# Performance work log

Hardware: AMD Instinct MI355X
Metric: run time of the kernel (lower is better)

Reference implementation:

```python
import jax, jax.numpy as jnp
import numpy as np

ALPHA = 0.9        # synaptic decay (hidden layers; layer 0 uses 0*syn + h)
BETA = 0.85        # membrane leak
THRESHOLD = 1.0
SIM_TIME = 50
SCALE = 100.0      # SurrGradSpike.scale


@jax.custom_vjp
def spike_fn(x):
    # Heaviside step: 1.0 where x > 0 (strict, matching torch `input > 0`)
    return (x > 0).astype(x.dtype)

def _spike_fwd(x):
    return spike_fn(x), x

def _spike_bwd(x, g):
    # normalized fast-sigmoid surrogate gradient (Zenke & Ganguli 2018)
    return (g / (SCALE * jnp.abs(x) + 1.0) ** 2,)

spike_fn.defvjp(_spike_fwd, _spike_bwd)


def setup_inputs() -> dict:
    key = jax.random.key(0)
    k0, k1, k2, k3 = jax.random.split(key, 4)
    return {
        "inputs": jax.random.normal(k0, (128, 1024), dtype=jnp.float32),
        "W0": jax.random.normal(k1, (1024, 2048), dtype=jnp.float32),
        "W1": jax.random.normal(k2, (2048, 2048), dtype=jnp.float32),
        "W2": jax.random.normal(k3, (2048, 512), dtype=jnp.float32),
    }


def _dsnn_forward(inputs, weights):
    batch = inputs.shape[0]
    n_layers = len(weights)
    syn0 = tuple(jnp.zeros((batch, W.shape[1]), dtype=inputs.dtype) for W in weights)
    mem0 = tuple(jnp.zeros((batch, W.shape[1]), dtype=inputs.dtype) for W in weights)

    def step(carry, _):
        syn, mem = carry
        new_syn, new_mem = [], []
        prev_spk = None
        for l, W in enumerate(weights):
            # feedforward drive: static input at layer 0, current-step spikes after
            h = inputs @ W if l == 0 else prev_spk @ W
            # layer 0: new_syn = 0*syn + h ; others: alpha*syn + h
            s = h if l == 0 else ALPHA * syn[l] + h
            m = BETA * mem[l] + s
            mthr = m - THRESHOLD
            out = spike_fn(mthr)
            if l < n_layers - 1:
                # hard reset to 0 where spiked (output layer never resets)
                m = jnp.where(mthr > 0, jnp.zeros_like(m), m)
            prev_spk = out
            new_syn.append(s)
            new_mem.append(m)
        return (tuple(new_syn), tuple(new_mem)), None

    (syn, mem), _ = jax.lax.scan(step, (syn0, mem0), None, length=SIM_TIME)
    # torch returns mem_rec[-1][-1]: output-layer membrane at final timestep
    return mem[-1]


def reference(inputs, W0, W1, W2):
    return _dsnn_forward(inputs, (W0, W1, W2))
```

## Files before the change

### kernel.cpp

```cpp
#include <hip/hip_runtime.h>
#include <hip/hip_bf16.h>

#define ALPHA 0.9f
#define BETA  0.85f
#define TSIM  50
#define BATCH 128
#define N0    1024
#define N1    2048
#define N2    2048
#define N3    512

#define A50   0.00515379f
#define B50   0.000295764f
#define INVAB 20.0f

typedef __attribute__((ext_vector_type(8))) short bf16x8;
typedef __attribute__((ext_vector_type(4))) float f32x4;

#define GLOBAL_AS __attribute__((address_space(1)))
#define LDS_AS    __attribute__((address_space(3)))

__global__ __launch_bounds__(256) void gemm_f32_splitk(const float* __restrict__ A,
                                                       const float* __restrict__ B,
                                                       float* __restrict__ Cp,
                                                       int M, int N, int K, int KC) {
    __shared__ float As[16][65];
    __shared__ float Bs[16][68];

    const int tid = threadIdx.x;
    const int tx  = tid % 16;
    const int ty  = tid / 16;
    const int bx  = blockIdx.x;
    const int by  = blockIdx.y;
    const int z   = blockIdx.z;

    float acc[4][4] = {};

    const int ar = tid / 4;
    const int ak = (tid % 4) * 4;
    const int br = tid / 16;
    const int bc = (tid % 16) * 4;

    const int kbeg = z * KC;
    for (int k0 = kbeg; k0 < kbeg + KC; k0 += 16) {
        float4 av = *(const float4*)&A[(size_t)(by * 64 + ar) * K + k0 + ak];
        As[ak + 0][ar] = av.x;
        As[ak + 1][ar] = av.y;
        As[ak + 2][ar] = av.z;
        As[ak + 3][ar] = av.w;
        float4 bv = *(const float4*)&B[(size_t)(k0 + br) * N + bx * 64 + bc];
        *(float4*)&Bs[br][bc] = bv;
        __syncthreads();

#pragma unroll
        for (int kk = 0; kk < 16; ++kk) {
            float a0 = As[kk][ty * 4 + 0];
            float a1 = As[kk][ty * 4 + 1];
            float a2 = As[kk][ty * 4 + 2];
            float a3 = As[kk][ty * 4 + 3];
            float b0 = Bs[kk][tx * 4 + 0];
            float b1 = Bs[kk][tx * 4 + 1];
            float b2 = Bs[kk][tx * 4 + 2];
            float b3 = Bs[kk][tx * 4 + 3];
            acc[0][0] += a0 * b0; acc[0][1] += a0 * b1; acc[0][2] += a0 * b2; acc[0][3] += a0 * b3;
            acc[1][0] += a1 * b0; acc[1][1] += a1 * b1; acc[1][2] += a1 * b2; acc[1][3] += a1 * b3;
            acc[2][0] += a2 * b0; acc[2][1] += a2 * b1; acc[2][2] += a2 * b2; acc[2][3] += a2 * b3;
            acc[3][0] += a3 * b0; acc[3][1] += a3 * b1; acc[3][2] += a3 * b2; acc[3][3] += a3 * b3;
        }
        __syncthreads();
    }

#pragma unroll
    for (int i = 0; i < 4; ++i) {
        float4 v = make_float4(acc[i][0], acc[i][1], acc[i][2], acc[i][3]);
        *(float4*)&Cp[((size_t)z * M + by * 64 + ty * 4 + i) * N + bx * 64 + tx * 4] = v;
    }
}

__global__ __launch_bounds__(256) void split_transpose(const float* __restrict__ W,
                                                       __hip_bfloat16* __restrict__ Th,
                                                       __hip_bfloat16* __restrict__ Tl,
                                                       int K, int N) {
    __shared__ float tile[32][33];
    const int tx = threadIdx.x % 32;
    const int ty = threadIdx.x / 32;
    const int k0 = blockIdx.y * 32;
    const int n0 = blockIdx.x * 32;

#pragma unroll
    for (int i = 0; i < 4; ++i)
        tile[ty + i * 8][tx] = W[(size_t)(k0 + ty + i * 8) * N + n0 + tx];
    __syncthreads();

#pragma unroll
    for (int i = 0; i < 4; ++i) {
        const float w = tile[tx][ty + i * 8];
        const __hip_bfloat16 hi = __float2bfloat16(w);
        const float lo = w - __bfloat162float(hi);
        const size_t o = (size_t)(n0 + ty + i * 8) * K + k0 + tx;
        Th[o] = hi;
        Tl[o] = __float2bfloat16(lo);
    }
}

template <int BN, int WGM, int WGN, int WMT, int WNT>
__global__ __launch_bounds__(256) void gemm_bf16_split_k(const __hip_bfloat16* __restrict__ A,
                                                         const __hip_bfloat16* __restrict__ Bh,
                                                         const __hip_bfloat16* __restrict__ Bl,
                                                         float* __restrict__ Cp,
                                                         int M, int N, int K, int KC) {
    constexpr int BM = 128;
    constexpr int BK = 32;
    constexpr int NA = (BM * BK) / (256 * 8);
    constexpr int NB = (BN * BK) / (256 * 8);

    __shared__ alignas(16) __hip_bfloat16 As[BM * BK];
    __shared__ alignas(16) __hip_bfloat16 Bhs[BN * BK];
    __shared__ alignas(16) __hip_bfloat16 Bls[BN * BK];

    const int tid  = threadIdx.x;
    const int wave = tid >> 6;
    const int lane = tid & 63;
    const int quad = lane >> 4;
    const int l16  = lane & 15;

    const int m0 = blockIdx.y * BM;
    const int n0 = blockIdx.x * BN;
    const int z  = blockIdx.z;

    const int wm = (wave % WGM) * (WMT * 16);
    const int wn = (wave / WGM) * (WNT * 16);

    f32x4 acc[WMT][WNT] = {};

    const __hip_bfloat16* agp[NA];
    int aoff[NA];
#pragma unroll
    for (int i = 0; i < NA; ++i) {
        const int c = i * 256 + tid;
        agp[i]  = A + (size_t)(m0 + (c >> 2)) * K + (c & 3) * 8;
        aoff[i] = c * 8;
    }
    const __hip_bfloat16 *bhgp[NB], *blgp[NB];
    int boff[NB];
#pragma unroll
    for (int i = 0; i < NB; ++i) {
        const int c = i * 256 + tid;
        bhgp[i] = Bh + (size_t)(n0 + (c >> 2)) * K + (c & 3) * 8;
        blgp[i] = Bl + (size_t)(n0 + (c >> 2)) * K + (c & 3) * 8;
        boff[i] = c * 8;
    }

    const int kbeg = z * KC;
    for (int k0 = kbeg; k0 < kbeg + KC; k0 += BK) {
#pragma unroll
        for (int i = 0; i < NA; ++i)
            __builtin_amdgcn_global_load_lds((const GLOBAL_AS void*)(agp[i] + k0),
                                             (LDS_AS void*)&As[aoff[i]], 16, 0, 0);
#pragma unroll
        for (int i = 0; i < NB; ++i) {
            __builtin_amdgcn_global_load_lds((const GLOBAL_AS void*)(bhgp[i] + k0),
                                             (LDS_AS void*)&Bhs[boff[i]], 16, 0, 0);
            __builtin_amdgcn_global_load_lds((const GLOBAL_AS void*)(blgp[i] + k0),
                                             (LDS_AS void*)&Bls[boff[i]], 16, 0, 0);
        }
        __syncthreads();

        bf16x8 af[WMT], bhf[WNT], blf[WNT];
#pragma unroll
        for (int i = 0; i < WMT; ++i)
            af[i] = *(const bf16x8*)&As[(wm + i * 16 + l16) * BK + quad * 8];
#pragma unroll
        for (int j = 0; j < WNT; ++j) {
            bhf[j] = *(const bf16x8*)&Bhs[(wn + j * 16 + l16) * BK + quad * 8];
            blf[j] = *(const bf16x8*)&Bls[(wn + j * 16 + l16) * BK + quad * 8];
        }
#pragma unroll
        for (int i = 0; i < WMT; ++i)
#pragma unroll
            for (int j = 0; j < WNT; ++j) {
                acc[i][j] = __builtin_amdgcn_mfma_f32_16x16x32_bf16(af[i], bhf[j], acc[i][j], 0, 0, 0);
                acc[i][j] = __builtin_amdgcn_mfma_f32_16x16x32_bf16(af[i], blf[j], acc[i][j], 0, 0, 0);
            }
        __syncthreads();
    }

#pragma unroll
    for (int i = 0; i < WMT; ++i)
#pragma unroll
        for (int j = 0; j < WNT; ++j)
#pragma unroll
            for (int r = 0; r < 4; ++r)
                Cp[((size_t)z * M + m0 + wm + i * 16 + quad * 4 + r) * N + n0 + wn + j * 16 + l16] =
                    acc[i][j][r];
}

__global__ __launch_bounds__(256) void scan_l0_classify(const float* __restrict__ P0,
                                                        __hip_bfloat16* __restrict__ C0,
                                                        int* __restrict__ jlist0,
                                                        unsigned long long* __restrict__ mask0,
                                                        int* __restrict__ count0) {
    const int b     = blockIdx.x;
    const int chunk = blockIdx.y;
    const int tid   = threadIdx.x;
    const int j     = chunk * 256 + tid;
    const int lane  = tid & 63;
    const int wv    = tid >> 6;

    float h = 0.f;
#pragma unroll
    for (int z = 0; z < 8; ++z) h += P0[((size_t)z * BATCH + b) * N1 + j];

    float m = 0.f;
    unsigned long long mask = 0ull;
#pragma unroll
    for (int t = 0; t < TSIM; ++t) {
        m = BETA * m + h;
        if (m - 1.f > 0.f) { mask |= (1ull << t); m = 0.f; }
    }
    const unsigned long long FULL = (1ull << TSIM) - 1ull;
    C0[(size_t)b * N1 + j] = __float2bfloat16((mask == FULL) ? 1.f : 0.f);

    const bool has = (mask != 0ull) && (mask != FULL);
    const unsigned long long bal = __ballot(has);

    __shared__ int wcnt[4];
    if (lane == 0) wcnt[wv] = __popcll(bal);
    __syncthreads();
    int base = 0;
#pragma unroll
    for (int w = 0; w < 4; ++w)
        if (w < wv) base += wcnt[w];
    const int pos = base + __popcll(bal & ((1ull << lane) - 1ull));

    const size_t lbase = (size_t)(b * 8 + chunk) * 256;
    if (has) {
        jlist0[lbase + pos] = j;
        mask0[lbase + pos]  = mask;
    }
    if (tid == 0) count0[b * 8 + chunk] = wcnt[0] + wcnt[1] + wcnt[2] + wcnt[3];
}

__global__ __launch_bounds__(256) void h1_scan_a2(const float* __restrict__ PB1,
                                                  const float* __restrict__ W1,
                                                  const int* __restrict__ jlist0,
                                                  const unsigned long long* __restrict__ mask0,
                                                  const int* __restrict__ count0,
                                                  float* __restrict__ A2) {
    const int b  = blockIdx.x;
    const int jc = blockIdx.y * 256 + threadIdx.x;

    float base = 0.f;
#pragma unroll
    for (int z = 0; z < 16; ++z) base += PB1[((size_t)z * BATCH + b) * N2 + jc];

    float s = 0.f, m = 0.f, a2 = 0.f;
    float pa = A50, pb = B50;
    const float inva = 1.0f / ALPHA, invb = 1.0f / BETA;

    float corr[25];

#pragma unroll
    for (int phase = 0; phase < 2; ++phase) {
        const int shift = phase * 25;

#pragma unroll
        for (int t = 0; t < 25; ++t) corr[t] = 0.f;

        for (int c = 0; c < 8; ++c) {
            const int cnt      = count0[b * 8 + c];
            const size_t lbase = (size_t)(b * 8 + c) * 256;
            for (int e = 0; e < cnt; ++e) {
                const unsigned mk = (unsigned)(mask0[lbase + e] >> shift);
                const int j       = jlist0[lbase + e];
                const float w     = W1[(size_t)j * N2 + jc];
#pragma unroll
                for (int t = 0; t < 25; ++t)
                    if ((mk >> t) & 1u) corr[t] += w;
            }
        }

#pragma unroll
        for (int t = 0; t < 25; ++t) {
            s = ALPHA * s + (base + corr[t]);
            m = BETA * m + s;
            if (m - 1.f > 0.f) {
                a2 += (pa - pb) * INVAB;
                m = 0.f;
            }
            pa *= inva;
            pb *= invb;
        }
    }
    A2[(size_t)b * N2 + jc] = a2;
}

__global__ __launch_bounds__(256) void reduce_out(const float* __restrict__ PB2,
                                                  float* __restrict__ out) {
    const int idx = blockIdx.x * 256 + threadIdx.x;
    float v = 0.f;
#pragma unroll
    for (int z = 0; z < 16; ++z) v += PB2[(size_t)z * (BATCH * N3) + idx];
    out[idx] = v;
}

extern "C" void kernel_launch(void* const* d_in, const int* in_sizes, int n_in,
                              void* d_out, int out_size, void* d_ws, size_t ws_size,
                              hipStream_t stream) {
    const float* inputs = (const float*)d_in[0];
    const float* W0     = (const float*)d_in[1];
    const float* W1     = (const float*)d_in[2];
    const float* W2     = (const float*)d_in[3];
    float* out = (float*)d_out;

    float* P0  = (float*)d_ws;
    float* PB1 = P0 + 8 * BATCH * N1;
    float* A2  = PB1 + 16 * BATCH * N2;
    float* PB2 = A2 + BATCH * N2;
    unsigned long long* mk0 = (unsigned long long*)(PB2 + 16 * BATCH * N3);
    __hip_bfloat16* C0bf = (__hip_bfloat16*)(mk0 + BATCH * 8 * 256);
    __hip_bfloat16* W1th = C0bf + (size_t)BATCH * N1;
    __hip_bfloat16* W1tl = W1th + (size_t)N2 * N1;
    int* jl0  = (int*)(W1tl + (size_t)N2 * N1);
    int* cnt0 = jl0 + BATCH * 8 * 256;

    split_transpose<<<dim3(N2 / 32, N1 / 32), 256, 0, stream>>>(W1, W1th, W1tl, N1, N2);

    gemm_f32_splitk<<<dim3(N1 / 64, BATCH / 64, 8), 256, 0, stream>>>(
        inputs, W0, P0, BATCH, N1, N0, N0 / 8);

    scan_l0_classify<<<dim3(BATCH, N1 / 256), 256, 0, stream>>>(P0, C0bf, jl0, mk0, cnt0);

    gemm_bf16_split_k<128, 2, 2, 4, 4>
        <<<dim3(N2 / 128, BATCH / 128, 16), 256, 0, stream>>>(
            C0bf, W1th, W1tl, PB1, BATCH, N2, N1, N1 / 16);

    h1_scan_a2<<<dim3(BATCH, N2 / 256), 256, 0, stream>>>(
        PB1, W1, jl0, mk0, cnt0, A2);

    gemm_f32_splitk<<<dim3(N3 / 64, BATCH / 64, 16), 256, 0, stream>>>(
        A2, W2, PB2, BATCH, N3, N2, N2 / 16);

    reduce_out<<<(BATCH * N3) / 256, 256, 0, stream>>>(PB2, out);
}
```

Measured before the change: 166.2 us.

## Replace split-K partial buffers with atomic accumulation and single-pass h1 correction scan

```diff
diff --git a/kernel.cpp b/kernel.cpp
--- a/kernel.cpp
+++ b/kernel.cpp
@@ -20,10 +20,17 @@
 #define GLOBAL_AS __attribute__((address_space(1)))
 #define LDS_AS    __attribute__((address_space(3)))
 
-__global__ __launch_bounds__(256) void gemm_f32_splitk(const float* __restrict__ A,
-                                                       const float* __restrict__ B,
-                                                       float* __restrict__ Cp,
-                                                       int M, int N, int K, int KC) {
+#define R32(X) X(0) X(1) X(2) X(3) X(4) X(5) X(6) X(7) X(8) X(9) X(10) X(11) \
+               X(12) X(13) X(14) X(15) X(16) X(17) X(18) X(19) X(20) X(21)   \
+               X(22) X(23) X(24) X(25) X(26) X(27) X(28) X(29) X(30) X(31)
+#define R18(X) X(32) X(33) X(34) X(35) X(36) X(37) X(38) X(39) X(40) X(41)   \
+               X(42) X(43) X(44) X(45) X(46) X(47) X(48) X(49)
+#define R50(X) R32(X) R18(X)
+
+__global__ __launch_bounds__(256) void gemm_f32_splitk_atomic(const float* __restrict__ A,
+                                                              const float* __restrict__ B,
+                                                              float* __restrict__ C,
+                                                              int M, int N, int K, int KC) {
     __shared__ float As[16][65];
     __shared__ float Bs[16][68];
 
@@ -71,10 +78,11 @@
     }
 
 #pragma unroll
-    for (int i = 0; i < 4; ++i) {
-        float4 v = make_float4(acc[i][0], acc[i][1], acc[i][2], acc[i][3]);
-        *(float4*)&Cp[((size_t)z * M + by * 64 + ty * 4 + i) * N + bx * 64 + tx * 4] = v;
-    }
+    for (int i = 0; i < 4; ++i)
+#pragma unroll
+        for (int jj = 0; jj < 4; ++jj)
+            atomicAdd(&C[(size_t)(by * 64 + ty * 4 + i) * N + bx * 64 + tx * 4 + jj],
+                      acc[i][jj]);
 }
 
 __global__ __launch_bounds__(256) void split_transpose(const float* __restrict__ W,
@@ -104,11 +112,12 @@
 }
 
 template <int BN, int WGM, int WGN, int WMT, int WNT>
-__global__ __launch_bounds__(256) void gemm_bf16_split_k(const __hip_bfloat16* __restrict__ A,
-                                                         const __hip_bfloat16* __restrict__ Bh,
-                                                         const __hip_bfloat16* __restrict__ Bl,
-                                                         float* __restrict__ Cp,
-                                                         int M, int N, int K, int KC) {
+__global__ __launch_bounds__(256) void gemm_bf16_split_k_atomic(
+        const __hip_bfloat16* __restrict__ A,
+        const __hip_bfloat16* __restrict__ Bh,
+        const __hip_bfloat16* __restrict__ Bl,
+        float* __restrict__ C,
+        int M, int N, int K, int KC) {
     constexpr int BM = 128;
     constexpr int BK = 32;
     constexpr int NA = (BM * BK) / (256 * 8);
@@ -191,11 +200,12 @@
         for (int j = 0; j < WNT; ++j)
 #pragma unroll
             for (int r = 0; r < 4; ++r)
-                Cp[((size_t)z * M + m0 + wm + i * 16 + quad * 4 + r) * N + n0 + wn + j * 16 + l16] =
-                    acc[i][j][r];
-}
-
-__global__ __launch_bounds__(256) void scan_l0_classify(const float* __restrict__ P0,
+                atomicAdd(&C[(size_t)(m0 + wm + i * 16 + quad * 4 + r) * N +
+                             n0 + wn + j * 16 + l16],
+                          acc[i][j][r]);
+}
+
+__global__ __launch_bounds__(256) void scan_l0_classify(const float* __restrict__ H0,
                                                         __hip_bfloat16* __restrict__ C0,
                                                         int* __restrict__ jlist0,
                                                         unsigned long long* __restrict__ mask0,
@@ -207,9 +217,7 @@
     const int lane  = tid & 63;
     const int wv    = tid >> 6;
 
-    float h = 0.f;
-#pragma unroll
-    for (int z = 0; z < 8; ++z) h += P0[((size_t)z * BATCH + b) * N1 + j];
+    const float h = H0[(size_t)b * N1 + j];
 
     float m = 0.f;
     unsigned long long mask = 0ull;
@@ -241,7 +249,7 @@
     if (tid == 0) count0[b * 8 + chunk] = wcnt[0] + wcnt[1] + wcnt[2] + wcnt[3];
 }
 
-__global__ __launch_bounds__(256) void h1_scan_a2(const float* __restrict__ PB1,
+__global__ __launch_bounds__(256) void h1_scan_a2(const float* __restrict__ H1,
                                                   const float* __restrict__ W1,
                                                   const int* __restrict__ jlist0,
                                                   const unsigned long long* __restrict__ mask0,
@@ -250,58 +258,42 @@
     const int b  = blockIdx.x;
     const int jc = blockIdx.y * 256 + threadIdx.x;
 
-    float base = 0.f;
-#pragma unroll
-    for (int z = 0; z < 16; ++z) base += PB1[((size_t)z * BATCH + b) * N2 + jc];
+    const float base = H1[(size_t)b * N2 + jc];
+
+#define DECL(t) float c##t = 0.f;
+    R50(DECL)
+#undef DECL
+
+    for (int c = 0; c < 8; ++c) {
+        const int cnt      = count0[b * 8 + c];
+        const size_t lbase = (size_t)(b * 8 + c) * 256;
+        for (int e = 0; e < cnt; ++e) {
+            const unsigned long long mk = mask0[lbase + e];
+            const int j                 = jlist0[lbase + e];
+            const float w               = W1[(size_t)j * N2 + jc];
+            const unsigned lo = (unsigned)mk, hi = (unsigned)(mk >> 32);
+#define PROBELO(t) c##t += (lo & (1u << (t))) ? w : 0.f;
+#define PROBEHI(t) c##t += (hi & (1u << ((t) - 32))) ? w : 0.f;
+            R32(PROBELO)
+            R18(PROBEHI)
+#undef PROBELO
+#undef PROBEHI
+        }
+    }
 
     float s = 0.f, m = 0.f, a2 = 0.f;
     float pa = A50, pb = B50;
     const float inva = 1.0f / ALPHA, invb = 1.0f / BETA;
-
-    float corr[25];
-
-#pragma unroll
-    for (int phase = 0; phase < 2; ++phase) {
-        const int shift = phase * 25;
-
-#pragma unroll
-        for (int t = 0; t < 25; ++t) corr[t] = 0.f;
-
-        for (int c = 0; c < 8; ++c) {
-            const int cnt      = count0[b * 8 + c];
-            const size_t lbase = (size_t)(b * 8 + c) * 256;
-            for (int e = 0; e < cnt; ++e) {
-                const unsigned mk = (unsigned)(mask0[lbase + e] >> shift);
-                const int j       = jlist0[lbase + e];
-                const float w     = W1[(size_t)j * N2 + jc];
-#pragma unroll
-                for (int t = 0; t < 25; ++t)
-                    if ((mk >> t) & 1u) corr[t] += w;
-            }
-        }
-
-#pragma unroll
-        for (int t = 0; t < 25; ++t) {
-            s = ALPHA * s + (base + corr[t]);
-            m = BETA * m + s;
-            if (m - 1.f > 0.f) {
-                a2 += (pa - pb) * INVAB;
-                m = 0.f;
-            }
-            pa *= inva;
-            pb *= invb;
-        }
-    }
+#define STEP(t)                                        \
+    s = ALPHA * s + (base + c##t);                     \
+    m = BETA * m + s;                                  \
+    if (m - 1.f > 0.f) { a2 += (pa - pb) * INVAB; m = 0.f; } \
+    pa *= inva;                                        \
+    pb *= invb;
+    R50(STEP)
+#undef STEP
+
     A2[(size_t)b * N2 + jc] = a2;
-}
-
-__global__ __launch_bounds__(256) void reduce_out(const float* __restrict__ PB2,
-                                                  float* __restrict__ out) {
-    const int idx = blockIdx.x * 256 + threadIdx.x;
-    float v = 0.f;
-#pragma unroll
-    for (int z = 0; z < 16; ++z) v += PB2[(size_t)z * (BATCH * N3) + idx];
-    out[idx] = v;
 }
 
 extern "C" void kernel_launch(void* const* d_in, const int* in_sizes, int n_in,
@@ -313,33 +305,33 @@
     const float* W2     = (const float*)d_in[3];
     float* out = (float*)d_out;
 
-    float* P0  = (float*)d_ws;
-    float* PB1 = P0 + 8 * BATCH * N1;
-    float* A2  = PB1 + 16 * BATCH * N2;
-    float* PB2 = A2 + BATCH * N2;
-    unsigned long long* mk0 = (unsigned long long*)(PB2 + 16 * BATCH * N3);
+    float* Hsum0 = (float*)d_ws;
+    float* Hsum1 = Hsum0 + BATCH * N1;
+    float* A2    = Hsum1 + BATCH * N2;
+    unsigned long long* mk0 = (unsigned long long*)(A2 + BATCH * N2);
     __hip_bfloat16* C0bf = (__hip_bfloat16*)(mk0 + BATCH * 8 * 256);
     __hip_bfloat16* W1th = C0bf + (size_t)BATCH * N1;
     __hip_bfloat16* W1tl = W1th + (size_t)N2 * N1;
     int* jl0  = (int*)(W1tl + (size_t)N2 * N1);
     int* cnt0 = jl0 + BATCH * 8 * 256;
 
+    hipMemsetAsync(Hsum0, 0, 2 * BATCH * N1 * sizeof(float), stream);
+    hipMemsetAsync(out, 0, (size_t)BATCH * N3 * sizeof(float), stream);
+
     split_transpose<<<dim3(N2 / 32, N1 / 32), 256, 0, stream>>>(W1, W1th, W1tl, N1, N2);
 
-    gemm_f32_splitk<<<dim3(N1 / 64, BATCH / 64, 8), 256, 0, stream>>>(
-        inputs, W0, P0, BATCH, N1, N0, N0 / 8);
-
-    scan_l0_classify<<<dim3(BATCH, N1 / 256), 256, 0, stream>>>(P0, C0bf, jl0, mk0, cnt0);
-
-    gemm_bf16_split_k<128, 2, 2, 4, 4>
+    gemm_f32_splitk_atomic<<<dim3(N1 / 64, BATCH / 64, 8), 256, 0, stream>>>(
+        inputs, W0, Hsum0, BATCH, N1, N0, N0 / 8);
+
+    scan_l0_classify<<<dim3(BATCH, N1 / 256), 256, 0, stream>>>(Hsum0, C0bf, jl0, mk0, cnt0);
+
+    gemm_bf16_split_k_atomic<128, 2, 2, 4, 4>
         <<<dim3(N2 / 128, BATCH / 128, 16), 256, 0, stream>>>(
-            C0bf, W1th, W1tl, PB1, BATCH, N2, N1, N1 / 16);
+            C0bf, W1th, W1tl, Hsum1, BATCH, N2, N1, N1 / 16);
 
     h1_scan_a2<<<dim3(BATCH, N2 / 256), 256, 0, stream>>>(
-        PB1, W1, jl0, mk0, cnt0, A2);
-
-    gemm_f32_splitk<<<dim3(N3 / 64, BATCH / 64, 16), 256, 0, stream>>>(
-        A2, W2, PB2, BATCH, N3, N2, N2 / 16);
-
-    reduce_out<<<(BATCH * N3) / 256, 256, 0, stream>>>(PB2, out);
-}
+        Hsum1, W1, jl0, mk0, cnt0, A2);
+
+    gemm_f32_splitk_atomic<<<dim3(N3 / 64, BATCH / 64, 16), 256, 0, stream>>>(
+        A2, W2, out, BATCH, N3, N2, N2 / 16);
+}
```

After: 215.9 us. +29.9%, slower.
